# Kernel tuning notes

Hardware: AMD Instinct MI355X
Metric: run time of the kernel (lower is better)

## Reference

```python
import jax, jax.numpy as jnp
import numpy as np

B, N, IN_F, OUT_F, H = 8, 1024, 128, 128, 4
HD = OUT_F // H  # 32
NEG_SLOPE = 0.2


def setup_inputs() -> dict:
    key = jax.random.key(0)
    k1, k2, k3, k4 = jax.random.split(key, 4)
    x = jax.random.normal(k1, (B, N, IN_F), dtype=jnp.float32)
    W = jax.random.normal(k2, (IN_F, OUT_F), dtype=jnp.float32) * (1.0 / np.sqrt(IN_F))
    a_src = jax.random.normal(k3, (H, HD), dtype=jnp.float32)
    a_dst = jax.random.normal(k4, (H, HD), dtype=jnp.float32)
    return {"x": x, "W": W, "a_src": a_src, "a_dst": a_dst}


def reference(x, W, a_src, a_dst):
    # Linear projection, split heads: (B, N, H, HD)
    h = (x @ W).reshape(B, N, H, HD)
    # Per-node additive attention terms: (B, N, H)
    attn_src = jnp.einsum("bnhd,hd->bnh", h, a_src)
    attn_dst = jnp.einsum("bnhd,hd->bnh", h, a_dst)
    # attn[b,i,j,h] = src_i + dst_j  -> (B, N, N, H)
    attn = attn_src[:, :, None, :] + attn_dst[:, None, :, :]
    attn = jnp.where(attn >= 0, attn, NEG_SLOPE * attn)  # LeakyReLU(0.2)
    attn = jax.nn.softmax(attn, axis=2)  # softmax over source nodes j
    # dropout is identity in eval/reference mode
    # Weighted aggregation per head: out[b,i,h,d] = sum_j attn[b,i,j,h] * h[b,j,h,d]
    out = jnp.einsum("bijh,bjhd->bihd", attn, h)
    return out.reshape(B, N, OUT_F)
```

## Files before the change

### kernel.cpp

```cpp
#include <hip/hip_runtime.h>


constexpr int CB  = 8;
constexpr int CN  = 1024;
constexpr int CF  = 128;
constexpr int CH  = 4;
constexpr int CHD = 32;
constexpr int CBH = CB * CH;
constexpr int CROWS = CB * CN;
constexpr int TROWS = CN + 1;
constexpr int NBK = 1024;

__global__ __launch_bounds__(256) void proj_kernel(
    const float* __restrict__ x, const float* __restrict__ W,
    const float* __restrict__ a_src, const float* __restrict__ a_dst,
    float* __restrict__ h_ws, float* __restrict__ sarr, float* __restrict__ darr)
{
    __shared__ float xs[8 * 132];
    __shared__ float wslab[64 * 128];

    const int tid = threadIdx.x, row0 = blockIdx.x * 8;

    {
        const int rr = tid >> 5, k4 = tid & 31;
        *(float4*)(xs + rr * 132 + k4 * 4) = ((const float4*)x)[(size_t)row0 * 32 + tid];
    }

    const int r = tid >> 5, c4 = tid & 31;
    const int head = c4 >> 3, dd0 = (c4 & 7) * 4;
    float acc[4] = {0.f, 0.f, 0.f, 0.f};

    const float4* W4 = (const float4*)W;
    for (int slab = 0; slab < 2; ++slab) {
        __syncthreads();
        #pragma unroll
        for (int m = 0; m < 8; ++m) {
            const int idx = m * 256 + tid;
            const int kk = idx >> 5, k4 = idx & 31;
            *(float4*)(wslab + kk * 128 + k4 * 4) = W4[(size_t)(slab * 64 + kk) * 32 + k4];
        }
        __syncthreads();
        #pragma unroll 4
        for (int k4 = 0; k4 < 16; ++k4) {
            const float4 xv = *(const float4*)(xs + r * 132 + slab * 64 + k4 * 4);
            const float xq[4] = {xv.x, xv.y, xv.z, xv.w};
            #pragma unroll
            for (int q = 0; q < 4; ++q) {
                const int kk = k4 * 4 + q;
                const float4 wv = *(const float4*)(wslab + kk * 128 + c4 * 4);
                const float xk = xq[q];
                acc[0] += xk * wv.x; acc[1] += xk * wv.y;
                acc[2] += xk * wv.z; acc[3] += xk * wv.w;
            }
        }
    }

    const float4 as = *(const float4*)(a_src + head * CHD + dd0);
    const float4 ad = *(const float4*)(a_dst + head * CHD + dd0);
    float sp = acc[0]*as.x + acc[1]*as.y + acc[2]*as.z + acc[3]*as.w;
    float dp = acc[0]*ad.x + acc[1]*ad.y + acc[2]*ad.z + acc[3]*ad.w;
    sp += __shfl_xor(sp, 1); sp += __shfl_xor(sp, 2); sp += __shfl_xor(sp, 4);
    dp += __shfl_xor(dp, 1); dp += __shfl_xor(dp, 2); dp += __shfl_xor(dp, 4);

    const int rowg = row0 + r, b = rowg >> 10, n = rowg & 1023;
    const int bh = b * CH + head;
    *(float4*)(h_ws + (size_t)(bh * CN + n) * CHD + dd0) =
        make_float4(acc[0], acc[1], acc[2], acc[3]);
    if ((c4 & 7) == 0) {
        sarr[bh * CN + n] = sp;
        darr[bh * CN + n] = dp;
    }
}

__global__ __launch_bounds__(1024) void count_kernel(
    const float* __restrict__ darr, float* __restrict__ dsrt_g,
    int* __restrict__ pj_g, int* __restrict__ bs_g, float* __restrict__ prm_g,
    float* __restrict__ sPB_g, float* __restrict__ sSF_g, float* __restrict__ tbl_g)
{
    __shared__ int   cnts[NBK];
    __shared__ int   startsS[NBK];
    __shared__ float redS[32];
    __shared__ int   wsumS[16];
    __shared__ float prmS[2];

    const int bh = blockIdx.x, tid = threadIdx.x;
    const int lane = tid & 63, wid = tid >> 6;

    const float d = darr[bh * CN + tid];

    float mn = d, mx = d;
    #pragma unroll
    for (int off = 1; off < 64; off <<= 1) {
        mn = fminf(mn, __shfl_xor(mn, off));
        mx = fmaxf(mx, __shfl_xor(mx, off));
    }
    if (lane == 0) { redS[wid] = mn; redS[16 + wid] = mx; }
    cnts[tid] = 0;
    __syncthreads();
    if (tid == 0) {
        float m0 = redS[0], m1 = redS[16];
        for (int w = 1; w < 16; ++w) { m0 = fminf(m0, redS[w]); m1 = fmaxf(m1, redS[16 + w]); }
        const float rng = fmaxf(m1 - m0, 1e-30f);
        const float invw = (float)NBK / rng;
        prmS[0] = m0; prmS[1] = invw;
        prm_g[bh * 2] = m0; prm_g[bh * 2 + 1] = invw;
    }
    __syncthreads();
    const float mnb = prmS[0], invw = prmS[1];
    const int f = (int)fminf(fmaxf((d - mnb) * invw, 0.0f), 1023.0f);
    const int rank = atomicAdd(&cnts[f], 1);
    __syncthreads();

    const int c = cnts[tid];
    int incl = c;
    #pragma unroll
    for (int off = 1; off < 64; off <<= 1) {
        const int t = __shfl_up(incl, off);
        if (lane >= off) incl += t;
    }
    if (lane == 63) wsumS[wid] = incl;
    __syncthreads();
    if (tid < 16) {
        const int v = wsumS[tid];
        int iv = v;
        #pragma unroll
        for (int off = 1; off < 16; off <<= 1) {
            const int t = __shfl_up(iv, off);
            if (tid >= off) iv += t;
        }
        wsumS[tid] = iv - v;
    }
    __syncthreads();
    const int excl = incl - c + wsumS[wid];
    startsS[tid] = excl;
    bs_g[bh * (NBK + 1) + tid] = excl;
    __syncthreads();

    const int pos = startsS[f] + rank;
    dsrt_g[bh * CN + pos] = d;
    pj_g[bh * CN + pos]   = tid;

    if (tid == 0) {
        bs_g[bh * (NBK + 1) + NBK] = CN;
        sPB_g[bh * TROWS + CN] = 0.f;
        sSF_g[bh * TROWS + CN] = 0.f;
    }
    if (tid < 64) tbl_g[(size_t)bh * TROWS * 64 + (size_t)CN * 64 + tid] = 0.f;
}

__global__ __launch_bounds__(256) void scan_kernel(
    const float* __restrict__ h_ws, const float* __restrict__ dsrt_g,
    const int* __restrict__ pj_g, float* __restrict__ tbl_g,
    float* __restrict__ sPB_g, float* __restrict__ sSF_g,
    float* __restrict__ ctF_g, float* __restrict__ ctB_g,
    float* __restrict__ ctSF_g, float* __restrict__ ctSB_g)
{
    __shared__ float dch[128];
    __shared__ int   pch[128];
    const int bh = blockIdx.x & 31, cg = blockIdx.x >> 5;
    const int tid = threadIdx.x, base = cg * 128;

    if (tid < 128) dch[tid] = dsrt_g[bh * CN + base + tid];
    else           pch[tid - 128] = pj_g[bh * CN + base + (tid - 128)];
    __syncthreads();

    const int dir = tid >> 7, cidx = (tid >> 5) & 3, dd = tid & 31;
    const int c = cg * 4 + cidx, lb = cidx * 32;
    const float* hb = h_ws + (size_t)bh * CN * CHD;
    float* tbl = tbl_g + (size_t)bh * TROWS * 64;

    if (dir == 0) {
        float accF = 0.f, accS = 0.f;
        for (int bt = 0; bt < 2; ++bt) {
            float hv[16], dv[16];
            #pragma unroll
            for (int t = 0; t < 16; ++t) {
                const int lp = lb + bt * 16 + t;
                hv[t] = hb[(size_t)pch[lp] * CHD + dd];
                dv[t] = dch[lp];
            }
            #pragma unroll
            for (int t = 0; t < 16; ++t) {
                const int pos = base + lb + bt * 16 + t;
                const float cf = __expf(0.2f * dv[t]);
                tbl[pos * 64 + dd] = accF;
                if (dd == 0) sPB_g[bh * TROWS + pos] = accS;
                accF += cf * hv[t];
                accS += cf;
            }
        }
        ctF_g[(bh * 32 + c) * 32 + dd] = accF;
        if (dd == 0) ctSF_g[bh * 32 + c] = accS;
    } else {
        float accB = 0.f, accS = 0.f;
        for (int bt = 0; bt < 2; ++bt) {
            float hv[16], dv[16];
            #pragma unroll
            for (int t = 0; t < 16; ++t) {
                const int lp = lb + 31 - (bt * 16 + t);
                hv[t] = hb[(size_t)pch[lp] * CHD + dd];
                dv[t] = dch[lp];
            }
            #pragma unroll
            for (int t = 0; t < 16; ++t) {
                const int pos = base + lb + 31 - (bt * 16 + t);
                const float cf = __expf(dv[t]);
                accB += cf * hv[t];
                accS += cf;
                tbl[pos * 64 + 32 + dd] = accB;
                if (dd == 0) sSF_g[bh * TROWS + pos] = accS;
            }
        }
        ctB_g[(bh * 32 + c) * 32 + dd] = accB;
        if (dd == 0) ctSB_g[bh * 32 + c] = accS;
    }
}

__global__ __launch_bounds__(256) void out_kernel(
    const float* __restrict__ h_ws, const float* __restrict__ sarr,
    const float* __restrict__ dsrt_g, const int* __restrict__ pj_g,
    const int* __restrict__ bs_g, const float* __restrict__ prm_g,
    const float* __restrict__ sPB_g, const float* __restrict__ sSF_g,
    const float* __restrict__ ctF_g, const float* __restrict__ ctB_g,
    const float* __restrict__ ctSF_g, const float* __restrict__ ctSB_g,
    const float* __restrict__ tbl_g, float* __restrict__ out)
{
    __shared__ float dsS[CN];
    __shared__ int   pjS[CN];
    __shared__ int   bsS[NBK + 1];
    __shared__ float ctF[32 * 32], ctB[32 * 32];
    __shared__ float ctSF[32], ctSB[32];
    __shared__ float ofF[33 * 32], ofB[33 * 32];
    __shared__ float ofSF[33], ofSB[33];

    const int bh = blockIdx.x & 31, q = blockIdx.x >> 5;
    const int tid = threadIdx.x;

    #pragma unroll
    for (int rr = 0; rr < 4; ++rr) {
        const int idx = rr * 256 + tid;
        dsS[idx] = dsrt_g[bh * CN + idx];
        pjS[idx] = pj_g[bh * CN + idx];
        bsS[idx] = bs_g[bh * (NBK + 1) + idx];
        ctF[idx] = ctF_g[bh * 1024 + idx];
        ctB[idx] = ctB_g[bh * 1024 + idx];
    }
    if (tid == 0) bsS[NBK] = bs_g[bh * (NBK + 1) + NBK];
    if (tid < 32)       ctSF[tid] = ctSF_g[bh * 32 + tid];
    else if (tid < 64)  ctSB[tid - 32] = ctSB_g[bh * 32 + (tid - 32)];
    __syncthreads();

    if (tid < 32) {
        float run = 0.f;
        for (int c = 0; c < 32; ++c) { ofF[c * 32 + tid] = run; run += ctF[c * 32 + tid]; }
        ofF[32 * 32 + tid] = run;
    } else if (tid < 64) {
        const int dd = tid - 32;
        float run = 0.f;
        ofB[32 * 32 + dd] = 0.f;
        for (int c = 31; c >= 0; --c) { ofB[c * 32 + dd] = run; run += ctB[c * 32 + dd]; }
    } else if (tid == 64) {
        float run = 0.f;
        for (int c = 0; c < 32; ++c) { ofSF[c] = run; run += ctSF[c]; }
        ofSF[32] = run;
    } else if (tid == 65) {
        float run = 0.f;
        ofSB[32] = 0.f;
        for (int c = 31; c >= 0; --c) { ofSB[c] = run; run += ctSB[c]; }
    }
    __syncthreads();

    const int i = q * 256 + tid;
    const float s = sarr[bh * CN + i];
    const float c1 = __expf(s), c2v = __expf(0.2f * s), thr = -s;
    const float mnb = prm_g[bh * 2], invw = prm_g[bh * 2 + 1];
    const int kb = (int)fminf(fmaxf((thr - mnb) * invw, 0.0f), 1023.0f);
    const int q0 = bsS[kb], q1 = bsS[kb + 1];
    const int kcf = q0 >> 5, kcb = q1 >> 5;

    float pbs = sPB_g[bh * TROWS + q0] + ofSF[kcf];
    float sfs = sSF_g[bh * TROWS + q1] + ofSB[kcb];

    const float4* trf = (const float4*)(tbl_g + (size_t)bh * TROWS * 64 + (size_t)q0 * 64);
    const float4* trb = (const float4*)(tbl_g + (size_t)bh * TROWS * 64 + (size_t)q1 * 64 + 32);
    float4 vF[8], vB[8];
    #pragma unroll
    for (int qq = 0; qq < 8; ++qq) {
        const float4 pb = trf[qq], oa = *(const float4*)(&ofF[kcf * 32 + qq * 4]);
        const float4 sf = trb[qq], ob = *(const float4*)(&ofB[kcb * 32 + qq * 4]);
        vF[qq] = make_float4(pb.x + oa.x, pb.y + oa.y, pb.z + oa.z, pb.w + oa.w);
        vB[qq] = make_float4(sf.x + ob.x, sf.y + ob.y, sf.z + ob.z, sf.w + ob.w);
    }

    const float* hb = h_ws + (size_t)bh * CN * CHD;
    for (int p = q0; p < q1; ++p) {
        const float dq = dsS[p];
        const float4* hr = (const float4*)(hb + (size_t)pjS[p] * CHD);
        const bool pre = (dq < thr);
        const float w = __expf(pre ? 0.2f * dq : dq);
        if (pre) pbs += w; else sfs += w;
        #pragma unroll
        for (int qq = 0; qq < 8; ++qq) {
            const float4 hv = hr[qq];
            if (pre) {
                vF[qq].x += w * hv.x; vF[qq].y += w * hv.y;
                vF[qq].z += w * hv.z; vF[qq].w += w * hv.w;
            } else {
                vB[qq].x += w * hv.x; vB[qq].y += w * hv.y;
                vB[qq].z += w * hv.z; vB[qq].w += w * hv.w;
            }
        }
    }

    const float inv = 1.0f / (c2v * pbs + c1 * sfs);
    const int b = bh >> 2, hh = bh & 3;
    float4* o = (float4*)(out + (size_t)(b * CN + i) * CF + hh * 32);
    #pragma unroll
    for (int qq = 0; qq < 8; ++qq) {
        o[qq] = make_float4((c2v * vF[qq].x + c1 * vB[qq].x) * inv,
                            (c2v * vF[qq].y + c1 * vB[qq].y) * inv,
                            (c2v * vF[qq].z + c1 * vB[qq].z) * inv,
                            (c2v * vF[qq].w + c1 * vB[qq].w) * inv);
    }
}

extern "C" void kernel_launch(void* const* d_in, const int* in_sizes, int n_in,
                              void* d_out, int out_size, void* d_ws, size_t ws_size,
                              hipStream_t stream) {
    const float* x     = (const float*)d_in[0];
    const float* W     = (const float*)d_in[1];
    const float* a_src = (const float*)d_in[2];
    const float* a_dst = (const float*)d_in[3];
    float* out = (float*)d_out;

    char* ws = (char*)d_ws;
    size_t off = 0;
    float* h_ws = (float*)(ws + off); off += (size_t)CROWS * CF * 4;
    float* sarr = (float*)(ws + off); off += (size_t)CBH * CN * 4;
    float* darr = (float*)(ws + off); off += (size_t)CBH * CN * 4;
    float* tblg = (float*)(ws + off); off += (size_t)CBH * TROWS * 64 * 4;
    float* dsrt = (float*)(ws + off); off += (size_t)CBH * CN * 4;
    int*   pjg  = (int*)  (ws + off); off += (size_t)CBH * CN * 4;
    float* sPBg = (float*)(ws + off); off += (size_t)CBH * TROWS * 4;
    float* sSFg = (float*)(ws + off); off += (size_t)CBH * TROWS * 4;
    float* ctFg = (float*)(ws + off); off += (size_t)CBH * 32 * 32 * 4;
    float* ctBg = (float*)(ws + off); off += (size_t)CBH * 32 * 32 * 4;
    float* ctSFg= (float*)(ws + off); off += (size_t)CBH * 32 * 4;
    float* ctSBg= (float*)(ws + off); off += (size_t)CBH * 32 * 4;
    int*   bsg  = (int*)  (ws + off); off += (size_t)CBH * (NBK + 1) * 4;
    float* prmg = (float*)(ws + off); off += (size_t)CBH * 2 * 4;
    (void)ws_size;

    proj_kernel<<<CROWS / 8, 256, 0, stream>>>(x, W, a_src, a_dst, h_ws, sarr, darr);
    count_kernel<<<CBH, 1024, 0, stream>>>(darr, dsrt, pjg, bsg, prmg, sPBg, sSFg, tblg);
    scan_kernel<<<256, 256, 0, stream>>>(h_ws, dsrt, pjg, tblg, sPBg, sSFg,
                                         ctFg, ctBg, ctSFg, ctSBg);
    out_kernel<<<128, 256, 0, stream>>>(h_ws, sarr, dsrt, pjg, bsg, prmg,
                                        sPBg, sSFg, ctFg, ctBg, ctSFg, ctSBg, tblg, out);
}
```

Measured before the change: 94.23 us.

## Fuse count, scan and output kernels into one per-head block kernel

Merges the bucket-sort count kernel, the chunked prefix-scan kernel and the output kernel into one tail_kernel with one 1024-thread block per (batch, head). Sorted keys, permutation, bucket starts, chunk totals and scalar prefix sums now stay in shared memory instead of round-tripping through global workspace. This removes two kernel launches and several global writes and reads. In exchange the scan and output phases run on only 32 blocks instead of 256 and 128, so far fewer CUs are used and each thread handles both scan directions one after the other.

```diff
diff --git a/kernel.cpp b/kernel.cpp
--- a/kernel.cpp
+++ b/kernel.cpp
@@ -72,22 +72,28 @@
     }
 }
 
-__global__ __launch_bounds__(1024) void count_kernel(
-    const float* __restrict__ darr, float* __restrict__ dsrt_g,
-    int* __restrict__ pj_g, int* __restrict__ bs_g, float* __restrict__ prm_g,
-    float* __restrict__ sPB_g, float* __restrict__ sSF_g, float* __restrict__ tbl_g)
+__global__ __launch_bounds__(1024) void tail_kernel(
+    const float* __restrict__ h_ws, const float* __restrict__ sarr,
+    const float* __restrict__ darr, float* __restrict__ tbl_g,
+    float* __restrict__ out)
 {
+    __shared__ float dchS[CN];
+    __shared__ int   pchS[CN];
+    __shared__ int   bsS[NBK + 1];
     __shared__ int   cnts[NBK];
-    __shared__ int   startsS[NBK];
+    __shared__ float ctF[32 * 32], ctB[32 * 32];
+    __shared__ float ofF[33 * 32], ofB[33 * 32];
+    __shared__ float ctSF[32], ctSB[32], ofSF[33], ofSB[33];
+    __shared__ float sPBl[CN + 1], sSFl[CN + 1];
     __shared__ float redS[32];
     __shared__ int   wsumS[16];
     __shared__ float prmS[2];
 
     const int bh = blockIdx.x, tid = threadIdx.x;
     const int lane = tid & 63, wid = tid >> 6;
+    float* tbl = tbl_g + (size_t)bh * TROWS * 64;
 
     const float d = darr[bh * CN + tid];
-
     float mn = d, mx = d;
     #pragma unroll
     for (int off = 1; off < 64; off <<= 1) {
@@ -96,14 +102,14 @@
     }
     if (lane == 0) { redS[wid] = mn; redS[16 + wid] = mx; }
     cnts[tid] = 0;
+    if (tid < 64) tbl[(size_t)CN * 64 + tid] = 0.f;
+    if (tid == 0) { sPBl[CN] = 0.f; sSFl[CN] = 0.f; }
     __syncthreads();
     if (tid == 0) {
         float m0 = redS[0], m1 = redS[16];
         for (int w = 1; w < 16; ++w) { m0 = fminf(m0, redS[w]); m1 = fmaxf(m1, redS[16 + w]); }
         const float rng = fmaxf(m1 - m0, 1e-30f);
-        const float invw = (float)NBK / rng;
-        prmS[0] = m0; prmS[1] = invw;
-        prm_g[bh * 2] = m0; prm_g[bh * 2 + 1] = invw;
+        prmS[0] = m0; prmS[1] = (float)NBK / rng;
     }
     __syncthreads();
     const float mnb = prmS[0], invw = prmS[1];
@@ -131,158 +137,96 @@
         wsumS[tid] = iv - v;
     }
     __syncthreads();
-    const int excl = incl - c + wsumS[wid];
-    startsS[tid] = excl;
-    bs_g[bh * (NBK + 1) + tid] = excl;
-    __syncthreads();
-
-    const int pos = startsS[f] + rank;
-    dsrt_g[bh * CN + pos] = d;
-    pj_g[bh * CN + pos]   = tid;
-
-    if (tid == 0) {
-        bs_g[bh * (NBK + 1) + NBK] = CN;
-        sPB_g[bh * TROWS + CN] = 0.f;
-        sSF_g[bh * TROWS + CN] = 0.f;
-    }
-    if (tid < 64) tbl_g[(size_t)bh * TROWS * 64 + (size_t)CN * 64 + tid] = 0.f;
-}
-
-__global__ __launch_bounds__(256) void scan_kernel(
-    const float* __restrict__ h_ws, const float* __restrict__ dsrt_g,
-    const int* __restrict__ pj_g, float* __restrict__ tbl_g,
-    float* __restrict__ sPB_g, float* __restrict__ sSF_g,
-    float* __restrict__ ctF_g, float* __restrict__ ctB_g,
-    float* __restrict__ ctSF_g, float* __restrict__ ctSB_g)
-{
-    __shared__ float dch[128];
-    __shared__ int   pch[128];
-    const int bh = blockIdx.x & 31, cg = blockIdx.x >> 5;
-    const int tid = threadIdx.x, base = cg * 128;
-
-    if (tid < 128) dch[tid] = dsrt_g[bh * CN + base + tid];
-    else           pch[tid - 128] = pj_g[bh * CN + base + (tid - 128)];
-    __syncthreads();
-
-    const int dir = tid >> 7, cidx = (tid >> 5) & 3, dd = tid & 31;
-    const int c = cg * 4 + cidx, lb = cidx * 32;
+    bsS[tid] = incl - c + wsumS[wid];
+    if (tid == 0) bsS[NBK] = CN;
+    __syncthreads();
+    const int pos = bsS[f] + rank;
+    dchS[pos] = d;
+    pchS[pos] = tid;
+    __syncthreads();
+
+    const int cc = tid >> 5, dd = tid & 31, cb = cc * 32;
     const float* hb = h_ws + (size_t)bh * CN * CHD;
-    float* tbl = tbl_g + (size_t)bh * TROWS * 64;
-
-    if (dir == 0) {
+    {
         float accF = 0.f, accS = 0.f;
         for (int bt = 0; bt < 2; ++bt) {
             float hv[16], dv[16];
             #pragma unroll
             for (int t = 0; t < 16; ++t) {
-                const int lp = lb + bt * 16 + t;
-                hv[t] = hb[(size_t)pch[lp] * CHD + dd];
-                dv[t] = dch[lp];
-            }
-            #pragma unroll
-            for (int t = 0; t < 16; ++t) {
-                const int pos = base + lb + bt * 16 + t;
+                const int lp = cb + bt * 16 + t;
+                hv[t] = hb[(size_t)pchS[lp] * CHD + dd];
+                dv[t] = dchS[lp];
+            }
+            #pragma unroll
+            for (int t = 0; t < 16; ++t) {
+                const int lp = cb + bt * 16 + t;
                 const float cf = __expf(0.2f * dv[t]);
-                tbl[pos * 64 + dd] = accF;
-                if (dd == 0) sPB_g[bh * TROWS + pos] = accS;
+                tbl[lp * 64 + dd] = accF;
+                if (dd == 0) sPBl[lp] = accS;
                 accF += cf * hv[t];
                 accS += cf;
             }
         }
-        ctF_g[(bh * 32 + c) * 32 + dd] = accF;
-        if (dd == 0) ctSF_g[bh * 32 + c] = accS;
-    } else {
+        ctF[cc * 32 + dd] = accF;
+        if (dd == 0) ctSF[cc] = accS;
+    }
+    {
         float accB = 0.f, accS = 0.f;
         for (int bt = 0; bt < 2; ++bt) {
             float hv[16], dv[16];
             #pragma unroll
             for (int t = 0; t < 16; ++t) {
-                const int lp = lb + 31 - (bt * 16 + t);
-                hv[t] = hb[(size_t)pch[lp] * CHD + dd];
-                dv[t] = dch[lp];
-            }
-            #pragma unroll
-            for (int t = 0; t < 16; ++t) {
-                const int pos = base + lb + 31 - (bt * 16 + t);
+                const int lp = cb + 31 - (bt * 16 + t);
+                hv[t] = hb[(size_t)pchS[lp] * CHD + dd];
+                dv[t] = dchS[lp];
+            }
+            #pragma unroll
+            for (int t = 0; t < 16; ++t) {
+                const int lp = cb + 31 - (bt * 16 + t);
                 const float cf = __expf(dv[t]);
                 accB += cf * hv[t];
                 accS += cf;
-                tbl[pos * 64 + 32 + dd] = accB;
-                if (dd == 0) sSF_g[bh * TROWS + pos] = accS;
-            }
-        }
-        ctB_g[(bh * 32 + c) * 32 + dd] = accB;
-        if (dd == 0) ctSB_g[bh * 32 + c] = accS;
-    }
-}
-
-__global__ __launch_bounds__(256) void out_kernel(
-    const float* __restrict__ h_ws, const float* __restrict__ sarr,
-    const float* __restrict__ dsrt_g, const int* __restrict__ pj_g,
-    const int* __restrict__ bs_g, const float* __restrict__ prm_g,
-    const float* __restrict__ sPB_g, const float* __restrict__ sSF_g,
-    const float* __restrict__ ctF_g, const float* __restrict__ ctB_g,
-    const float* __restrict__ ctSF_g, const float* __restrict__ ctSB_g,
-    const float* __restrict__ tbl_g, float* __restrict__ out)
-{
-    __shared__ float dsS[CN];
-    __shared__ int   pjS[CN];
-    __shared__ int   bsS[NBK + 1];
-    __shared__ float ctF[32 * 32], ctB[32 * 32];
-    __shared__ float ctSF[32], ctSB[32];
-    __shared__ float ofF[33 * 32], ofB[33 * 32];
-    __shared__ float ofSF[33], ofSB[33];
-
-    const int bh = blockIdx.x & 31, q = blockIdx.x >> 5;
-    const int tid = threadIdx.x;
-
-    #pragma unroll
-    for (int rr = 0; rr < 4; ++rr) {
-        const int idx = rr * 256 + tid;
-        dsS[idx] = dsrt_g[bh * CN + idx];
-        pjS[idx] = pj_g[bh * CN + idx];
-        bsS[idx] = bs_g[bh * (NBK + 1) + idx];
-        ctF[idx] = ctF_g[bh * 1024 + idx];
-        ctB[idx] = ctB_g[bh * 1024 + idx];
-    }
-    if (tid == 0) bsS[NBK] = bs_g[bh * (NBK + 1) + NBK];
-    if (tid < 32)       ctSF[tid] = ctSF_g[bh * 32 + tid];
-    else if (tid < 64)  ctSB[tid - 32] = ctSB_g[bh * 32 + (tid - 32)];
+                tbl[lp * 64 + 32 + dd] = accB;
+                if (dd == 0) sSFl[lp] = accS;
+            }
+        }
+        ctB[cc * 32 + dd] = accB;
+        if (dd == 0) ctSB[cc] = accS;
+    }
     __syncthreads();
 
     if (tid < 32) {
         float run = 0.f;
-        for (int c = 0; c < 32; ++c) { ofF[c * 32 + tid] = run; run += ctF[c * 32 + tid]; }
+        for (int c2 = 0; c2 < 32; ++c2) { ofF[c2 * 32 + tid] = run; run += ctF[c2 * 32 + tid]; }
         ofF[32 * 32 + tid] = run;
     } else if (tid < 64) {
-        const int dd = tid - 32;
-        float run = 0.f;
-        ofB[32 * 32 + dd] = 0.f;
-        for (int c = 31; c >= 0; --c) { ofB[c * 32 + dd] = run; run += ctB[c * 32 + dd]; }
+        const int d2 = tid - 32;
+        float run = 0.f;
+        ofB[32 * 32 + d2] = 0.f;
+        for (int c2 = 31; c2 >= 0; --c2) { ofB[c2 * 32 + d2] = run; run += ctB[c2 * 32 + d2]; }
     } else if (tid == 64) {
         float run = 0.f;
-        for (int c = 0; c < 32; ++c) { ofSF[c] = run; run += ctSF[c]; }
+        for (int c2 = 0; c2 < 32; ++c2) { ofSF[c2] = run; run += ctSF[c2]; }
         ofSF[32] = run;
     } else if (tid == 65) {
         float run = 0.f;
         ofSB[32] = 0.f;
-        for (int c = 31; c >= 0; --c) { ofSB[c] = run; run += ctSB[c]; }
-    }
-    __syncthreads();
-
-    const int i = q * 256 + tid;
+        for (int c2 = 31; c2 >= 0; --c2) { ofSB[c2] = run; run += ctSB[c2]; }
+    }
+    __syncthreads();
+
+    const int i = tid;
     const float s = sarr[bh * CN + i];
     const float c1 = __expf(s), c2v = __expf(0.2f * s), thr = -s;
-    const float mnb = prm_g[bh * 2], invw = prm_g[bh * 2 + 1];
     const int kb = (int)fminf(fmaxf((thr - mnb) * invw, 0.0f), 1023.0f);
     const int q0 = bsS[kb], q1 = bsS[kb + 1];
     const int kcf = q0 >> 5, kcb = q1 >> 5;
 
-    float pbs = sPB_g[bh * TROWS + q0] + ofSF[kcf];
-    float sfs = sSF_g[bh * TROWS + q1] + ofSB[kcb];
-
-    const float4* trf = (const float4*)(tbl_g + (size_t)bh * TROWS * 64 + (size_t)q0 * 64);
-    const float4* trb = (const float4*)(tbl_g + (size_t)bh * TROWS * 64 + (size_t)q1 * 64 + 32);
+    float pbs = sPBl[q0] + ofSF[kcf];
+    float sfs = sSFl[q1] + ofSB[kcb];
+
+    const float4* trf = (const float4*)(tbl + (size_t)q0 * 64);
+    const float4* trb = (const float4*)(tbl + (size_t)q1 * 64 + 32);
     float4 vF[8], vB[8];
     #pragma unroll
     for (int qq = 0; qq < 8; ++qq) {
@@ -292,10 +236,9 @@
         vB[qq] = make_float4(sf.x + ob.x, sf.y + ob.y, sf.z + ob.z, sf.w + ob.w);
     }
 
-    const float* hb = h_ws + (size_t)bh * CN * CHD;
     for (int p = q0; p < q1; ++p) {
-        const float dq = dsS[p];
-        const float4* hr = (const float4*)(hb + (size_t)pjS[p] * CHD);
+        const float dq = dchS[p];
+        const float4* hr = (const float4*)(hb + (size_t)pchS[p] * CHD);
         const bool pre = (dq < thr);
         const float w = __expf(pre ? 0.2f * dq : dq);
         if (pre) pbs += w; else sfs += w;
@@ -339,22 +282,8 @@
     float* sarr = (float*)(ws + off); off += (size_t)CBH * CN * 4;
     float* darr = (float*)(ws + off); off += (size_t)CBH * CN * 4;
     float* tblg = (float*)(ws + off); off += (size_t)CBH * TROWS * 64 * 4;
-    float* dsrt = (float*)(ws + off); off += (size_t)CBH * CN * 4;
-    int*   pjg  = (int*)  (ws + off); off += (size_t)CBH * CN * 4;
-    float* sPBg = (float*)(ws + off); off += (size_t)CBH * TROWS * 4;
-    float* sSFg = (float*)(ws + off); off += (size_t)CBH * TROWS * 4;
-    float* ctFg = (float*)(ws + off); off += (size_t)CBH * 32 * 32 * 4;
-    float* ctBg = (float*)(ws + off); off += (size_t)CBH * 32 * 32 * 4;
-    float* ctSFg= (float*)(ws + off); off += (size_t)CBH * 32 * 4;
-    float* ctSBg= (float*)(ws + off); off += (size_t)CBH * 32 * 4;
-    int*   bsg  = (int*)  (ws + off); off += (size_t)CBH * (NBK + 1) * 4;
-    float* prmg = (float*)(ws + off); off += (size_t)CBH * 2 * 4;
     (void)ws_size;
 
     proj_kernel<<<CROWS / 8, 256, 0, stream>>>(x, W, a_src, a_dst, h_ws, sarr, darr);
-    count_kernel<<<CBH, 1024, 0, stream>>>(darr, dsrt, pjg, bsg, prmg, sPBg, sSFg, tblg);
-    scan_kernel<<<256, 256, 0, stream>>>(h_ws, dsrt, pjg, tblg, sPBg, sSFg,
-                                         ctFg, ctBg, ctSFg, ctSBg);
-    out_kernel<<<128, 256, 0, stream>>>(h_ws, sarr, dsrt, pjg, bsg, prmg,
-                                        sPBg, sSFg, ctFg, ctBg, ctSFg, ctSBg, tblg, out);
+    tail_kernel<<<CBH, 1024, 0, stream>>>(h_ws, sarr, darr, tblg, out);
 }
```

After: 112.6 us. +19.5%, slower.

## Fuse four GAT stages into one cooperative kernel with grid syncs

Applied to the files above, without the earlier changes.

Merges the projection, bucket-count, scan and output kernels into one persistent cooperative kernel of 256 blocks, separated by grid.sync, and keeps the separate kernels as a fallback. To fit the uniform 256-block, 256-thread grid, each stage is reshaped: projection handles 32 rows per block, counting uses 256 threads with 4 elements each, and output splits each row's head dimension across two threads. The goal is to remove three launch gaps and raise output-stage parallelism. The cost is grid-barrier overhead and a shared-memory footprint sized for the largest stage, which may lower occupancy in the other stages.

```diff
diff --git a/kernel.cpp b/kernel.cpp
--- a/kernel.cpp
+++ b/kernel.cpp
@@ -1,4 +1,6 @@
 #include <hip/hip_runtime.h>
+#include <hip/hip_cooperative_groups.h>
+namespace cg = cooperative_groups;
 
 
 constexpr int CB  = 8;
@@ -10,25 +12,29 @@
 constexpr int CROWS = CB * CN;
 constexpr int TROWS = CN + 1;
 constexpr int NBK = 1024;
-
-__global__ __launch_bounds__(256) void proj_kernel(
+constexpr int BSST = 1028;
+constexpr int SMEM_BYTES = 49920;
+
+__device__ __forceinline__ void phase_proj(char* smem, int blk, int tid,
     const float* __restrict__ x, const float* __restrict__ W,
     const float* __restrict__ a_src, const float* __restrict__ a_dst,
     float* __restrict__ h_ws, float* __restrict__ sarr, float* __restrict__ darr)
 {
-    __shared__ float xs[8 * 132];
-    __shared__ float wslab[64 * 128];
-
-    const int tid = threadIdx.x, row0 = blockIdx.x * 8;
-
-    {
-        const int rr = tid >> 5, k4 = tid & 31;
-        *(float4*)(xs + rr * 132 + k4 * 4) = ((const float4*)x)[(size_t)row0 * 32 + tid];
-    }
-
-    const int r = tid >> 5, c4 = tid & 31;
+    float* xs    = (float*)smem;
+    float* wslab = (float*)(smem + 16896);
+
+    const int row0 = blk * 32;
+    const float4* x4 = (const float4*)x;
+    #pragma unroll
+    for (int m = 0; m < 4; ++m) {
+        const int idx = m * 256 + tid;
+        const int r = idx >> 5, k4 = idx & 31;
+        *(float4*)(xs + r * 132 + k4 * 4) = x4[(size_t)row0 * 32 + idx];
+    }
+
+    const int rr = tid >> 5, c4 = tid & 31;
     const int head = c4 >> 3, dd0 = (c4 & 7) * 4;
-    float acc[4] = {0.f, 0.f, 0.f, 0.f};
+    float acc[4][4] = {};
 
     const float4* W4 = (const float4*)W;
     for (int slab = 0; slab < 2; ++slab) {
@@ -40,79 +46,90 @@
             *(float4*)(wslab + kk * 128 + k4 * 4) = W4[(size_t)(slab * 64 + kk) * 32 + k4];
         }
         __syncthreads();
-        #pragma unroll 4
+        #pragma unroll 2
         for (int k4 = 0; k4 < 16; ++k4) {
-            const float4 xv = *(const float4*)(xs + r * 132 + slab * 64 + k4 * 4);
-            const float xq[4] = {xv.x, xv.y, xv.z, xv.w};
+            float xq[4][4];
+            #pragma unroll
+            for (int j = 0; j < 4; ++j) {
+                const float4 xv = *(const float4*)(xs + (rr + j * 8) * 132 + slab * 64 + k4 * 4);
+                xq[j][0] = xv.x; xq[j][1] = xv.y; xq[j][2] = xv.z; xq[j][3] = xv.w;
+            }
             #pragma unroll
             for (int q = 0; q < 4; ++q) {
-                const int kk = k4 * 4 + q;
-                const float4 wv = *(const float4*)(wslab + kk * 128 + c4 * 4);
-                const float xk = xq[q];
-                acc[0] += xk * wv.x; acc[1] += xk * wv.y;
-                acc[2] += xk * wv.z; acc[3] += xk * wv.w;
+                const float4 wv = *(const float4*)(wslab + (k4 * 4 + q) * 128 + c4 * 4);
+                #pragma unroll
+                for (int j = 0; j < 4; ++j) {
+                    acc[j][0] += xq[j][q] * wv.x; acc[j][1] += xq[j][q] * wv.y;
+                    acc[j][2] += xq[j][q] * wv.z; acc[j][3] += xq[j][q] * wv.w;
+                }
             }
         }
     }
 
     const float4 as = *(const float4*)(a_src + head * CHD + dd0);
     const float4 ad = *(const float4*)(a_dst + head * CHD + dd0);
-    float sp = acc[0]*as.x + acc[1]*as.y + acc[2]*as.z + acc[3]*as.w;
-    float dp = acc[0]*ad.x + acc[1]*ad.y + acc[2]*ad.z + acc[3]*ad.w;
-    sp += __shfl_xor(sp, 1); sp += __shfl_xor(sp, 2); sp += __shfl_xor(sp, 4);
-    dp += __shfl_xor(dp, 1); dp += __shfl_xor(dp, 2); dp += __shfl_xor(dp, 4);
-
-    const int rowg = row0 + r, b = rowg >> 10, n = rowg & 1023;
-    const int bh = b * CH + head;
-    *(float4*)(h_ws + (size_t)(bh * CN + n) * CHD + dd0) =
-        make_float4(acc[0], acc[1], acc[2], acc[3]);
-    if ((c4 & 7) == 0) {
-        sarr[bh * CN + n] = sp;
-        darr[bh * CN + n] = dp;
-    }
-}
-
-__global__ __launch_bounds__(1024) void count_kernel(
+    const int b = row0 >> 10, bh = b * CH + head;
+    #pragma unroll
+    for (int j = 0; j < 4; ++j) {
+        float sp = acc[j][0]*as.x + acc[j][1]*as.y + acc[j][2]*as.z + acc[j][3]*as.w;
+        float dp = acc[j][0]*ad.x + acc[j][1]*ad.y + acc[j][2]*ad.z + acc[j][3]*ad.w;
+        sp += __shfl_xor(sp, 1); sp += __shfl_xor(sp, 2); sp += __shfl_xor(sp, 4);
+        dp += __shfl_xor(dp, 1); dp += __shfl_xor(dp, 2); dp += __shfl_xor(dp, 4);
+        const int n = (row0 + rr + j * 8) & 1023;
+        *(float4*)(h_ws + ((size_t)bh * CN + n) * CHD + dd0) =
+            make_float4(acc[j][0], acc[j][1], acc[j][2], acc[j][3]);
+        if ((c4 & 7) == 0) { sarr[bh * CN + n] = sp; darr[bh * CN + n] = dp; }
+    }
+}
+
+__device__ __forceinline__ void phase_count(char* smem, int bh, int tid,
     const float* __restrict__ darr, float* __restrict__ dsrt_g,
     int* __restrict__ pj_g, int* __restrict__ bs_g, float* __restrict__ prm_g,
     float* __restrict__ sPB_g, float* __restrict__ sSF_g, float* __restrict__ tbl_g)
 {
-    __shared__ int   cnts[NBK];
-    __shared__ int   startsS[NBK];
-    __shared__ float redS[32];
-    __shared__ int   wsumS[16];
-    __shared__ float prmS[2];
-
-    const int bh = blockIdx.x, tid = threadIdx.x;
+    int*   cnts  = (int*)smem;
+    int*   bsS   = (int*)(smem + 4096);
+    float* redmn = (float*)(smem + 8208);
+    float* redmx = (float*)(smem + 8224);
+    int*   wsumS = (int*)(smem + 8240);
+    float* prmS  = (float*)(smem + 8260);
+
     const int lane = tid & 63, wid = tid >> 6;
-
-    const float d = darr[bh * CN + tid];
-
-    float mn = d, mx = d;
+    float dv[4];
+    #pragma unroll
+    for (int u = 0; u < 4; ++u) dv[u] = darr[bh * CN + tid + 256 * u];
+    float mn = fminf(fminf(dv[0], dv[1]), fminf(dv[2], dv[3]));
+    float mx = fmaxf(fmaxf(dv[0], dv[1]), fmaxf(dv[2], dv[3]));
     #pragma unroll
     for (int off = 1; off < 64; off <<= 1) {
         mn = fminf(mn, __shfl_xor(mn, off));
         mx = fmaxf(mx, __shfl_xor(mx, off));
     }
-    if (lane == 0) { redS[wid] = mn; redS[16 + wid] = mx; }
-    cnts[tid] = 0;
+    if (lane == 0) { redmn[wid] = mn; redmx[wid] = mx; }
+    #pragma unroll
+    for (int u = 0; u < 4; ++u) cnts[tid + 256 * u] = 0;
+    if (tid < 64) tbl_g[(size_t)bh * TROWS * 64 + (size_t)CN * 64 + tid] = 0.f;
     __syncthreads();
     if (tid == 0) {
-        float m0 = redS[0], m1 = redS[16];
-        for (int w = 1; w < 16; ++w) { m0 = fminf(m0, redS[w]); m1 = fmaxf(m1, redS[16 + w]); }
+        float m0 = fminf(fminf(redmn[0], redmn[1]), fminf(redmn[2], redmn[3]));
+        float m1 = fmaxf(fmaxf(redmx[0], redmx[1]), fmaxf(redmx[2], redmx[3]));
         const float rng = fmaxf(m1 - m0, 1e-30f);
-        const float invw = (float)NBK / rng;
-        prmS[0] = m0; prmS[1] = invw;
-        prm_g[bh * 2] = m0; prm_g[bh * 2 + 1] = invw;
+        prmS[0] = m0; prmS[1] = (float)NBK / rng;
+        prm_g[bh * 2] = m0; prm_g[bh * 2 + 1] = prmS[1];
+        sPB_g[bh * TROWS + CN] = 0.f; sSF_g[bh * TROWS + CN] = 0.f;
     }
     __syncthreads();
     const float mnb = prmS[0], invw = prmS[1];
-    const int f = (int)fminf(fmaxf((d - mnb) * invw, 0.0f), 1023.0f);
-    const int rank = atomicAdd(&cnts[f], 1);
-    __syncthreads();
-
-    const int c = cnts[tid];
-    int incl = c;
+    int fb[4], rk[4];
+    #pragma unroll
+    for (int u = 0; u < 4; ++u) {
+        fb[u] = (int)fminf(fmaxf((dv[u] - mnb) * invw, 0.0f), 1023.0f);
+        rk[u] = atomicAdd(&cnts[fb[u]], 1);
+    }
+    __syncthreads();
+    const int c0 = cnts[4*tid], c1 = cnts[4*tid+1], c2 = cnts[4*tid+2], c3 = cnts[4*tid+3];
+    const int sum4 = c0 + c1 + c2 + c3;
+    int incl = sum4;
     #pragma unroll
     for (int off = 1; off < 64; off <<= 1) {
         const int t = __shfl_up(incl, off);
@@ -120,45 +137,33 @@
     }
     if (lane == 63) wsumS[wid] = incl;
     __syncthreads();
-    if (tid < 16) {
-        const int v = wsumS[tid];
-        int iv = v;
-        #pragma unroll
-        for (int off = 1; off < 16; off <<= 1) {
-            const int t = __shfl_up(iv, off);
-            if (tid >= off) iv += t;
-        }
-        wsumS[tid] = iv - v;
-    }
-    __syncthreads();
-    const int excl = incl - c + wsumS[wid];
-    startsS[tid] = excl;
-    bs_g[bh * (NBK + 1) + tid] = excl;
-    __syncthreads();
-
-    const int pos = startsS[f] + rank;
-    dsrt_g[bh * CN + pos] = d;
-    pj_g[bh * CN + pos]   = tid;
-
-    if (tid == 0) {
-        bs_g[bh * (NBK + 1) + NBK] = CN;
-        sPB_g[bh * TROWS + CN] = 0.f;
-        sSF_g[bh * TROWS + CN] = 0.f;
-    }
-    if (tid < 64) tbl_g[(size_t)bh * TROWS * 64 + (size_t)CN * 64 + tid] = 0.f;
-}
-
-__global__ __launch_bounds__(256) void scan_kernel(
+    if (tid == 0) { int r0 = 0; for (int w = 0; w < 4; ++w) { const int t = wsumS[w]; wsumS[w] = r0; r0 += t; } }
+    __syncthreads();
+    const int base = incl - sum4 + wsumS[wid];
+    const int b0 = base, b1 = base + c0, b2 = base + c0 + c1, b3 = base + c0 + c1 + c2;
+    bsS[4*tid] = b0; bsS[4*tid+1] = b1; bsS[4*tid+2] = b2; bsS[4*tid+3] = b3;
+    *(int4*)(bs_g + (size_t)bh * BSST + 4 * tid) = make_int4(b0, b1, b2, b3);
+    if (tid == 0) { bsS[NBK] = CN; bs_g[(size_t)bh * BSST + NBK] = CN; }
+    __syncthreads();
+    #pragma unroll
+    for (int u = 0; u < 4; ++u) {
+        const int pos = bsS[fb[u]] + rk[u];
+        dsrt_g[bh * CN + pos] = dv[u];
+        pj_g[bh * CN + pos]   = tid + 256 * u;
+    }
+}
+
+__device__ __forceinline__ void phase_scan(char* smem, int blk, int tid,
     const float* __restrict__ h_ws, const float* __restrict__ dsrt_g,
     const int* __restrict__ pj_g, float* __restrict__ tbl_g,
     float* __restrict__ sPB_g, float* __restrict__ sSF_g,
     float* __restrict__ ctF_g, float* __restrict__ ctB_g,
     float* __restrict__ ctSF_g, float* __restrict__ ctSB_g)
 {
-    __shared__ float dch[128];
-    __shared__ int   pch[128];
-    const int bh = blockIdx.x & 31, cg = blockIdx.x >> 5;
-    const int tid = threadIdx.x, base = cg * 128;
+    float* dch = (float*)smem;
+    int*   pch = (int*)(smem + 512);
+    const int bh = blk & 31, cg = blk >> 5;
+    const int base = cg * 128;
 
     if (tid < 128) dch[tid] = dsrt_g[bh * CN + base + tid];
     else           pch[tid - 128] = pj_g[bh * CN + base + (tid - 128)];
@@ -216,7 +221,7 @@
     }
 }
 
-__global__ __launch_bounds__(256) void out_kernel(
+__device__ __forceinline__ void phase_out(char* smem, int blk, int tid,
     const float* __restrict__ h_ws, const float* __restrict__ sarr,
     const float* __restrict__ dsrt_g, const int* __restrict__ pj_g,
     const int* __restrict__ bs_g, const float* __restrict__ prm_g,
@@ -225,52 +230,55 @@
     const float* __restrict__ ctSF_g, const float* __restrict__ ctSB_g,
     const float* __restrict__ tbl_g, float* __restrict__ out)
 {
-    __shared__ float dsS[CN];
-    __shared__ int   pjS[CN];
-    __shared__ int   bsS[NBK + 1];
-    __shared__ float ctF[32 * 32], ctB[32 * 32];
-    __shared__ float ctSF[32], ctSB[32];
-    __shared__ float ofF[33 * 32], ofB[33 * 32];
-    __shared__ float ofSF[33], ofSB[33];
-
-    const int bh = blockIdx.x & 31, q = blockIdx.x >> 5;
-    const int tid = threadIdx.x;
+    float* dsS  = (float*)smem;
+    int*   pjS  = (int*)(smem + 4096);
+    int*   bsS  = (int*)(smem + 8192);
+    float* ctF  = (float*)(smem + 12304);
+    float* ctB  = (float*)(smem + 16400);
+    float* ofF  = (float*)(smem + 20496);
+    float* ofB  = (float*)(smem + 24720);
+    float* ctSF = (float*)(smem + 28944);
+    float* ctSB = (float*)(smem + 29072);
+    float* ofSF = (float*)(smem + 29200);
+    float* ofSB = (float*)(smem + 29344);
+
+    const int bh = blk & 31, oct = blk >> 5;
 
     #pragma unroll
     for (int rr = 0; rr < 4; ++rr) {
         const int idx = rr * 256 + tid;
         dsS[idx] = dsrt_g[bh * CN + idx];
         pjS[idx] = pj_g[bh * CN + idx];
-        bsS[idx] = bs_g[bh * (NBK + 1) + idx];
+        bsS[idx] = bs_g[(size_t)bh * BSST + idx];
         ctF[idx] = ctF_g[bh * 1024 + idx];
         ctB[idx] = ctB_g[bh * 1024 + idx];
     }
-    if (tid == 0) bsS[NBK] = bs_g[bh * (NBK + 1) + NBK];
-    if (tid < 32)       ctSF[tid] = ctSF_g[bh * 32 + tid];
-    else if (tid < 64)  ctSB[tid - 32] = ctSB_g[bh * 32 + (tid - 32)];
+    if (tid == 0) bsS[NBK] = CN;
+    if (tid < 32)      ctSF[tid] = ctSF_g[bh * 32 + tid];
+    else if (tid < 64) ctSB[tid - 32] = ctSB_g[bh * 32 + (tid - 32)];
     __syncthreads();
 
     if (tid < 32) {
         float run = 0.f;
-        for (int c = 0; c < 32; ++c) { ofF[c * 32 + tid] = run; run += ctF[c * 32 + tid]; }
+        for (int c2 = 0; c2 < 32; ++c2) { ofF[c2 * 32 + tid] = run; run += ctF[c2 * 32 + tid]; }
         ofF[32 * 32 + tid] = run;
     } else if (tid < 64) {
-        const int dd = tid - 32;
+        const int d2 = tid - 32;
         float run = 0.f;
-        ofB[32 * 32 + dd] = 0.f;
-        for (int c = 31; c >= 0; --c) { ofB[c * 32 + dd] = run; run += ctB[c * 32 + dd]; }
+        ofB[32 * 32 + d2] = 0.f;
+        for (int c2 = 31; c2 >= 0; --c2) { ofB[c2 * 32 + d2] = run; run += ctB[c2 * 32 + d2]; }
     } else if (tid == 64) {
         float run = 0.f;
-        for (int c = 0; c < 32; ++c) { ofSF[c] = run; run += ctSF[c]; }
+        for (int c2 = 0; c2 < 32; ++c2) { ofSF[c2] = run; run += ctSF[c2]; }
         ofSF[32] = run;
     } else if (tid == 65) {
         float run = 0.f;
         ofSB[32] = 0.f;
-        for (int c = 31; c >= 0; --c) { ofSB[c] = run; run += ctSB[c]; }
-    }
-    __syncthreads();
-
-    const int i = q * 256 + tid;
+        for (int c2 = 31; c2 >= 0; --c2) { ofSB[c2] = run; run += ctSB[c2]; }
+    }
+    __syncthreads();
+
+    const int i = oct * 128 + (tid >> 1), half = tid & 1, hd0 = half * 16;
     const float s = sarr[bh * CN + i];
     const float c1 = __expf(s), c2v = __expf(0.2f * s), thr = -s;
     const float mnb = prm_g[bh * 2], invw = prm_g[bh * 2 + 1];
@@ -281,13 +289,14 @@
     float pbs = sPB_g[bh * TROWS + q0] + ofSF[kcf];
     float sfs = sSF_g[bh * TROWS + q1] + ofSB[kcb];
 
-    const float4* trf = (const float4*)(tbl_g + (size_t)bh * TROWS * 64 + (size_t)q0 * 64);
-    const float4* trb = (const float4*)(tbl_g + (size_t)bh * TROWS * 64 + (size_t)q1 * 64 + 32);
-    float4 vF[8], vB[8];
-    #pragma unroll
-    for (int qq = 0; qq < 8; ++qq) {
-        const float4 pb = trf[qq], oa = *(const float4*)(&ofF[kcf * 32 + qq * 4]);
-        const float4 sf = trb[qq], ob = *(const float4*)(&ofB[kcb * 32 + qq * 4]);
+    const float* tb = tbl_g + (size_t)bh * TROWS * 64;
+    const float4* trf = (const float4*)(tb + (size_t)q0 * 64 + hd0);
+    const float4* trb = (const float4*)(tb + (size_t)q1 * 64 + 32 + hd0);
+    float4 vF[4], vB[4];
+    #pragma unroll
+    for (int qq = 0; qq < 4; ++qq) {
+        const float4 pb = trf[qq], oa = *(const float4*)(&ofF[kcf * 32 + hd0 + qq * 4]);
+        const float4 sf = trb[qq], ob = *(const float4*)(&ofB[kcb * 32 + hd0 + qq * 4]);
         vF[qq] = make_float4(pb.x + oa.x, pb.y + oa.y, pb.z + oa.z, pb.w + oa.w);
         vB[qq] = make_float4(sf.x + ob.x, sf.y + ob.y, sf.z + ob.z, sf.w + ob.w);
     }
@@ -295,33 +304,96 @@
     const float* hb = h_ws + (size_t)bh * CN * CHD;
     for (int p = q0; p < q1; ++p) {
         const float dq = dsS[p];
-        const float4* hr = (const float4*)(hb + (size_t)pjS[p] * CHD);
+        const float4* hr = (const float4*)(hb + (size_t)pjS[p] * CHD + hd0);
         const bool pre = (dq < thr);
         const float w = __expf(pre ? 0.2f * dq : dq);
         if (pre) pbs += w; else sfs += w;
         #pragma unroll
-        for (int qq = 0; qq < 8; ++qq) {
+        for (int qq = 0; qq < 4; ++qq) {
             const float4 hv = hr[qq];
-            if (pre) {
-                vF[qq].x += w * hv.x; vF[qq].y += w * hv.y;
-                vF[qq].z += w * hv.z; vF[qq].w += w * hv.w;
-            } else {
-                vB[qq].x += w * hv.x; vB[qq].y += w * hv.y;
-                vB[qq].z += w * hv.z; vB[qq].w += w * hv.w;
-            }
+            if (pre) { vF[qq].x += w*hv.x; vF[qq].y += w*hv.y; vF[qq].z += w*hv.z; vF[qq].w += w*hv.w; }
+            else     { vB[qq].x += w*hv.x; vB[qq].y += w*hv.y; vB[qq].z += w*hv.z; vB[qq].w += w*hv.w; }
         }
     }
 
     const float inv = 1.0f / (c2v * pbs + c1 * sfs);
     const int b = bh >> 2, hh = bh & 3;
-    float4* o = (float4*)(out + (size_t)(b * CN + i) * CF + hh * 32);
-    #pragma unroll
-    for (int qq = 0; qq < 8; ++qq) {
+    float4* o = (float4*)(out + (size_t)(b * CN + i) * CF + hh * 32 + hd0);
+    #pragma unroll
+    for (int qq = 0; qq < 4; ++qq) {
         o[qq] = make_float4((c2v * vF[qq].x + c1 * vB[qq].x) * inv,
                             (c2v * vF[qq].y + c1 * vB[qq].y) * inv,
                             (c2v * vF[qq].z + c1 * vB[qq].z) * inv,
                             (c2v * vF[qq].w + c1 * vB[qq].w) * inv);
     }
+}
+
+__global__ __launch_bounds__(256) void gat_fused(
+    const float* __restrict__ x, const float* __restrict__ W,
+    const float* __restrict__ a_src, const float* __restrict__ a_dst,
+    float* __restrict__ h_ws, float* __restrict__ sarr, float* __restrict__ darr,
+    float* __restrict__ dsrt_g, int* __restrict__ pj_g, int* __restrict__ bs_g,
+    float* __restrict__ prm_g, float* __restrict__ sPB_g, float* __restrict__ sSF_g,
+    float* __restrict__ ctF_g, float* __restrict__ ctB_g,
+    float* __restrict__ ctSF_g, float* __restrict__ ctSB_g,
+    float* __restrict__ tbl_g, float* __restrict__ out)
+{
+    __shared__ __align__(16) char smem[SMEM_BYTES];
+    cg::grid_group grid = cg::this_grid();
+    const int tid = threadIdx.x, blk = blockIdx.x;
+
+    phase_proj(smem, blk, tid, x, W, a_src, a_dst, h_ws, sarr, darr);
+    grid.sync();
+    if (blk < CBH)
+        phase_count(smem, blk, tid, darr, dsrt_g, pj_g, bs_g, prm_g, sPB_g, sSF_g, tbl_g);
+    grid.sync();
+    phase_scan(smem, blk, tid, h_ws, dsrt_g, pj_g, tbl_g, sPB_g, sSF_g,
+               ctF_g, ctB_g, ctSF_g, ctSB_g);
+    grid.sync();
+    phase_out(smem, blk, tid, h_ws, sarr, dsrt_g, pj_g, bs_g, prm_g, sPB_g, sSF_g,
+              ctF_g, ctB_g, ctSF_g, ctSB_g, tbl_g, out);
+}
+
+__global__ __launch_bounds__(256) void k_proj(
+    const float* __restrict__ x, const float* __restrict__ W,
+    const float* __restrict__ a_src, const float* __restrict__ a_dst,
+    float* __restrict__ h_ws, float* __restrict__ sarr, float* __restrict__ darr)
+{
+    __shared__ __align__(16) char smem[SMEM_BYTES];
+    phase_proj(smem, blockIdx.x, threadIdx.x, x, W, a_src, a_dst, h_ws, sarr, darr);
+}
+__global__ __launch_bounds__(256) void k_count(
+    const float* __restrict__ darr, float* __restrict__ dsrt_g, int* __restrict__ pj_g,
+    int* __restrict__ bs_g, float* __restrict__ prm_g,
+    float* __restrict__ sPB_g, float* __restrict__ sSF_g, float* __restrict__ tbl_g)
+{
+    __shared__ __align__(16) char smem[SMEM_BYTES];
+    phase_count(smem, blockIdx.x, threadIdx.x, darr, dsrt_g, pj_g, bs_g, prm_g,
+                sPB_g, sSF_g, tbl_g);
+}
+__global__ __launch_bounds__(256) void k_scan(
+    const float* __restrict__ h_ws, const float* __restrict__ dsrt_g,
+    const int* __restrict__ pj_g, float* __restrict__ tbl_g,
+    float* __restrict__ sPB_g, float* __restrict__ sSF_g,
+    float* __restrict__ ctF_g, float* __restrict__ ctB_g,
+    float* __restrict__ ctSF_g, float* __restrict__ ctSB_g)
+{
+    __shared__ __align__(16) char smem[SMEM_BYTES];
+    phase_scan(smem, blockIdx.x, threadIdx.x, h_ws, dsrt_g, pj_g, tbl_g, sPB_g, sSF_g,
+               ctF_g, ctB_g, ctSF_g, ctSB_g);
+}
+__global__ __launch_bounds__(256) void k_out(
+    const float* __restrict__ h_ws, const float* __restrict__ sarr,
+    const float* __restrict__ dsrt_g, const int* __restrict__ pj_g,
+    const int* __restrict__ bs_g, const float* __restrict__ prm_g,
+    const float* __restrict__ sPB_g, const float* __restrict__ sSF_g,
+    const float* __restrict__ ctF_g, const float* __restrict__ ctB_g,
+    const float* __restrict__ ctSF_g, const float* __restrict__ ctSB_g,
+    const float* __restrict__ tbl_g, float* __restrict__ out)
+{
+    __shared__ __align__(16) char smem[SMEM_BYTES];
+    phase_out(smem, blockIdx.x, threadIdx.x, h_ws, sarr, dsrt_g, pj_g, bs_g, prm_g,
+              sPB_g, sSF_g, ctF_g, ctB_g, ctSF_g, ctSB_g, tbl_g, out);
 }
 
 extern "C" void kernel_launch(void* const* d_in, const int* in_sizes, int n_in,
@@ -341,20 +413,31 @@
     float* tblg = (float*)(ws + off); off += (size_t)CBH * TROWS * 64 * 4;
     float* dsrt = (float*)(ws + off); off += (size_t)CBH * CN * 4;
     int*   pjg  = (int*)  (ws + off); off += (size_t)CBH * CN * 4;
+    int*   bsg  = (int*)  (ws + off); off += (size_t)CBH * BSST * 4;
+    float* prmg = (float*)(ws + off); off += (size_t)CBH * 2 * 4;
     float* sPBg = (float*)(ws + off); off += (size_t)CBH * TROWS * 4;
     float* sSFg = (float*)(ws + off); off += (size_t)CBH * TROWS * 4;
     float* ctFg = (float*)(ws + off); off += (size_t)CBH * 32 * 32 * 4;
     float* ctBg = (float*)(ws + off); off += (size_t)CBH * 32 * 32 * 4;
     float* ctSFg= (float*)(ws + off); off += (size_t)CBH * 32 * 4;
     float* ctSBg= (float*)(ws + off); off += (size_t)CBH * 32 * 4;
-    int*   bsg  = (int*)  (ws + off); off += (size_t)CBH * (NBK + 1) * 4;
-    float* prmg = (float*)(ws + off); off += (size_t)CBH * 2 * 4;
     (void)ws_size;
 
-    proj_kernel<<<CROWS / 8, 256, 0, stream>>>(x, W, a_src, a_dst, h_ws, sarr, darr);
-    count_kernel<<<CBH, 1024, 0, stream>>>(darr, dsrt, pjg, bsg, prmg, sPBg, sSFg, tblg);
-    scan_kernel<<<256, 256, 0, stream>>>(h_ws, dsrt, pjg, tblg, sPBg, sSFg,
-                                         ctFg, ctBg, ctSFg, ctSBg);
-    out_kernel<<<128, 256, 0, stream>>>(h_ws, sarr, dsrt, pjg, bsg, prmg,
-                                        sPBg, sSFg, ctFg, ctBg, ctSFg, ctSBg, tblg, out);
-}
+    void* args[] = {
+        (void*)&x, (void*)&W, (void*)&a_src, (void*)&a_dst,
+        (void*)&h_ws, (void*)&sarr, (void*)&darr,
+        (void*)&dsrt, (void*)&pjg, (void*)&bsg, (void*)&prmg,
+        (void*)&sPBg, (void*)&sSFg, (void*)&ctFg, (void*)&ctBg,
+        (void*)&ctSFg, (void*)&ctSBg, (void*)&tblg, (void*)&out
+    };
+    const hipError_t e = hipLaunchCooperativeKernel(
+        (const void*)gat_fused, dim3(256), dim3(256), args, 0, stream);
+    if (e != hipSuccess) {
+        k_proj<<<256, 256, 0, stream>>>(x, W, a_src, a_dst, h_ws, sarr, darr);
+        k_count<<<CBH, 256, 0, stream>>>(darr, dsrt, pjg, bsg, prmg, sPBg, sSFg, tblg);
+        k_scan<<<256, 256, 0, stream>>>(h_ws, dsrt, pjg, tblg, sPBg, sSFg,
+                                        ctFg, ctBg, ctSFg, ctSBg);
+        k_out<<<256, 256, 0, stream>>>(h_ws, sarr, dsrt, pjg, bsg, prmg,
+                                       sPBg, sSFg, ctFg, ctBg, ctSFg, ctSBg, tblg, out);
+    }
+}
```

New measurement: 175.6 us. +86.4%, slower.
